# Kernel optimization log

Measured on AMD Instinct MI355X. Metric: run time of the kernel, lower is better.

The kernel has to match this reference:

```python
import jax, jax.numpy as jnp
import numpy as np

D_MODEL = 1024; D_STATE = 128; D_CONV = 4; EXPAND = 2; HEADDIM = 64; NGROUPS = 1
CHUNK = 256; B_SZ = 2; SEQ = 4096
D_INNER = EXPAND * D_MODEL
NHEADS = D_INNER // HEADDIM
CONV_DIM = D_INNER + 2 * NGROUPS * D_STATE
D_IN_PROJ = 2 * D_INNER + 2 * NGROUPS * D_STATE + NHEADS
EPS = 1e-5


def setup_inputs() -> dict:
    key = jax.random.key(0)
    ks = jax.random.split(key, 12)
    # dt_bias init exactly as in the module (inverse-softplus of dt in [dt_min, dt_max])
    dt0 = jnp.exp(jax.random.uniform(ks[0], (NHEADS,)) * (np.log(0.1) - np.log(0.001)) + np.log(0.001))
    dt0 = jnp.clip(dt0, 1e-4)
    dt_bias = dt0 + jnp.log(-jnp.expm1(-dt0))
    A_log = jnp.log(jax.random.uniform(ks[1], (NHEADS,), minval=1.0, maxval=16.0))
    return {
        "u": jax.random.normal(ks[2], (B_SZ, SEQ, D_MODEL), jnp.float32),
        "delta_t": jax.random.uniform(ks[3], (B_SZ, SEQ, 1), jnp.float32),
        "W_in": jax.random.normal(ks[4], (D_IN_PROJ, D_MODEL), jnp.float32) / np.sqrt(D_MODEL),
        "conv_w": jax.random.normal(ks[5], (CONV_DIM, D_CONV), jnp.float32) * 0.2,
        "conv_b": jax.random.normal(ks[6], (CONV_DIM,), jnp.float32) * 0.02,
        "dt_bias": dt_bias,
        "gamma": jax.random.uniform(ks[7], (NHEADS,)),
        "A_log": A_log,
        "D": jnp.ones((NHEADS,), jnp.float32),
        "norm_w": jnp.ones((D_INNER,), jnp.float32),
        "W_out": jax.random.normal(ks[8], (D_MODEL, D_INNER), jnp.float32) / np.sqrt(D_INNER),
    }


def _segsum(x):
    # x: (..., T) -> (..., T, T) masked lower-triangular segment sums
    T = x.shape[-1]
    cs = jnp.cumsum(x, axis=-1)
    seg = cs[..., :, None] - cs[..., None, :]
    mask = jnp.tril(jnp.ones((T, T), bool))
    return jnp.where(mask, seg, -jnp.inf)


def _forward(u, delta_t, W_in, conv_w, conv_b, dt_bias, gamma, A_log, D, norm_w, W_out):
    b, L, _ = u.shape
    zxbcdt = u @ W_in.T                               # (b, L, d_in_proj), d_mlp == 0
    z = zxbcdt[..., :D_INNER]
    xBC = zxbcdt[..., D_INNER:D_INNER + CONV_DIM]
    dt = zxbcdt[..., D_INNER + CONV_DIM:]             # (b, L, nheads)
    dt = dt + gamma[None, None, :] * delta_t          # time-scale-aware shift
    # causal depthwise conv1d (pad left d_conv-1) + SiLU
    xBC = jax.lax.conv_general_dilated(
        xBC.transpose(0, 2, 1), conv_w[:, None, :], (1,), [(D_CONV - 1, 0)],
        feature_group_count=CONV_DIM, dimension_numbers=("NCH", "OIH", "NCH"))
    xBC = jax.nn.silu(xBC.transpose(0, 2, 1) + conv_b)
    x = xBC[..., :D_INNER].reshape(b, L, NHEADS, HEADDIM)
    Bm = xBC[..., D_INNER:D_INNER + D_STATE]          # ngroups == 1 -> (b, L, n)
    Cm = xBC[..., D_INNER + D_STATE:]
    A = -jnp.exp(A_log)                               # (h,)
    dt = jax.nn.softplus(dt + dt_bias)                # dt_softplus=True, dt_limit=(0, inf)
    # ---- chunked SSD scan (mamba_chunk_scan_combined) ----
    c = L // CHUNK
    Xc = (x * dt[..., None]).reshape(b, c, CHUNK, NHEADS, HEADDIM)
    Ac = (dt * A).reshape(b, c, CHUNK, NHEADS).transpose(0, 3, 1, 2)    # (b,h,c,Q)
    Bc = Bm.reshape(b, c, CHUNK, D_STATE)
    Cc = Cm.reshape(b, c, CHUNK, D_STATE)
    A_cumsum = jnp.cumsum(Ac, axis=-1)                                   # (b,h,c,Q)
    Lmat = jnp.exp(_segsum(Ac))                                          # (b,h,c,Q,Q)
    # intra-chunk (diagonal blocks)
    Y_diag = jnp.einsum("bcqn,bckn,bhcqk,bckhp->bcqhp", Cc, Bc, Lmat, Xc)
    # per-chunk states at chunk ends
    decay_states = jnp.exp(A_cumsum[..., -1:] - A_cumsum)                # (b,h,c,Q)
    states = jnp.einsum("bckn,bhck,bckhp->bchpn", Bc, decay_states, Xc)
    # inter-chunk recurrence over chunk index
    chunk_decay = jnp.exp(A_cumsum[..., -1])                             # (b,h,c)

    def step(s, inp):
        dec, st = inp
        return dec[..., None, None] * s + st, s

    _, prev_states = jax.lax.scan(
        step,
        jnp.zeros((b, NHEADS, HEADDIM, D_STATE), Xc.dtype),
        (chunk_decay.transpose(2, 0, 1), states.transpose(1, 0, 2, 3, 4)))  # prev: (c,b,h,p,n)
    Y_off = jnp.einsum("bcqn,cbhpn,bhcq->bcqhp", Cc, prev_states, jnp.exp(A_cumsum))
    y = (Y_diag + Y_off).reshape(b, L, NHEADS, HEADDIM)
    y = y + x * D[None, None, :, None]                # skip connection D
    y = y.reshape(b, L, D_INNER)
    # gated RMSNorm (norm_before_gate=False): norm(y * silu(z)) * w, group_size = d_ssm
    yg = y * jax.nn.silu(z)
    yg = yg * jax.lax.rsqrt(jnp.mean(jnp.square(yg), axis=-1, keepdims=True) + EPS) * norm_w
    return yg @ W_out.T


def reference(u, delta_t, W_in, conv_w, conv_b, dt_bias, gamma, A_log, D, norm_w, W_out):
    return _forward(u, delta_t, W_in, conv_w, conv_b, dt_bias, gamma, A_log, D, norm_w, W_out)
```

## Files before the change

kernel.cpp:

```cpp
#include <hip/hip_runtime.h>
#include <hip/hip_bf16.h>
#include <math.h>

#define DM    1024
#define DIP   4384
#define NP1   4480
#define NPX   4352
#define DI    2048
#define CD    2304
#define NH    32
#define HD    64
#define DS    128
#define CH    256
#define NCH   16
#define BSZ   2
#define SEQ   4096
#define NTOK  (BSZ*SEQ)

typedef __bf16 bf16_t;
typedef __attribute__((ext_vector_type(8))) __bf16 bf16x8;
typedef __attribute__((ext_vector_type(4))) float f32x4;

__device__ __forceinline__ f32x4 mfma16(bf16x8 a, bf16x8 b, f32x4 c) {
    return __builtin_amdgcn_mfma_f32_16x16x32_bf16(a, b, c, 0, 0, 0);
}

__device__ __forceinline__ void gload_lds16(const bf16_t* g, bf16_t* l) {
    __builtin_amdgcn_global_load_lds(
        (const __attribute__((address_space(1))) unsigned int*)g,
        (__attribute__((address_space(3))) unsigned int*)l, 16, 0, 0);
}

__global__ void k_cvt(const float* __restrict__ in, bf16_t* __restrict__ out, int n) {
    int i = blockIdx.x * 256 + threadIdx.x;
    if (i < n) out[i] = (bf16_t)in[i];
}

__global__ void k_cvt_pad(const float* __restrict__ in, bf16_t* __restrict__ out) {
    int i = blockIdx.x * 256 + threadIdx.x;
    if (i >= NP1 * DM) return;
    int r = i >> 10;
    out[i] = (r < DIP) ? (bf16_t)in[i] : (bf16_t)0.f;
}

template <typename OutT>
__global__ __launch_bounds__(256) void k_gemm(const bf16_t* __restrict__ A,
                                              const bf16_t* __restrict__ Bt,
                                              OutT* __restrict__ C, int K, int ldc) {
    __shared__ __align__(16) bf16_t sA[128 * 32];
    __shared__ __align__(16) bf16_t sB[128 * 32];
    int tid = threadIdx.x, wave = tid >> 6, lane = tid & 63;
    int l15 = lane & 15, quad = lane >> 4;
    int m0 = blockIdx.y * 128, n0 = blockIdx.x * 128;
    int wm = (wave & 1) * 64, wn = (wave >> 1) * 64;
    f32x4 acc[4][4];
#pragma unroll
    for (int i = 0; i < 4; i++)
#pragma unroll
        for (int j = 0; j < 4; j++) acc[i][j] = (f32x4){0.f, 0.f, 0.f, 0.f};

    int srow = lane >> 2, scol = (lane & 3) * 8;
    const bf16_t* Ag0 = A + (size_t)(m0 + wave * 32 + srow) * K + scol;
    const bf16_t* Ag1 = Ag0 + (size_t)16 * K;
    const bf16_t* Bg0 = Bt + (size_t)(n0 + wave * 32 + srow) * K + scol;
    const bf16_t* Bg1 = Bg0 + (size_t)16 * K;
    bf16_t* lA0 = sA + (wave * 32) * 32;
    bf16_t* lA1 = sA + (wave * 32 + 16) * 32;
    bf16_t* lB0 = sB + (wave * 32) * 32;
    bf16_t* lB1 = sB + (wave * 32 + 16) * 32;

    for (int k0 = 0; k0 < K; k0 += 32) {
        gload_lds16(Ag0 + k0, lA0);
        gload_lds16(Ag1 + k0, lA1);
        gload_lds16(Bg0 + k0, lB0);
        gload_lds16(Bg1 + k0, lB1);
        __syncthreads();
        bf16x8 af[4], bg[4];
#pragma unroll
        for (int mt = 0; mt < 4; mt++) af[mt] = *(const bf16x8*)&sA[(wm + mt * 16 + l15) * 32 + quad * 8];
#pragma unroll
        for (int nt = 0; nt < 4; nt++) bg[nt] = *(const bf16x8*)&sB[(wn + nt * 16 + l15) * 32 + quad * 8];
#pragma unroll
        for (int mt = 0; mt < 4; mt++)
#pragma unroll
            for (int nt = 0; nt < 4; nt++)
                acc[mt][nt] = mfma16(af[mt], bg[nt], acc[mt][nt]);
        __syncthreads();
    }
#pragma unroll
    for (int mt = 0; mt < 4; mt++)
#pragma unroll
        for (int nt = 0; nt < 4; nt++)
#pragma unroll
            for (int r = 0; r < 4; r++)
                C[(size_t)(m0 + wm + mt * 16 + quad * 4 + r) * ldc + n0 + wn + nt * 16 + l15] =
                    (OutT)acc[mt][nt][r];
}

__global__ __launch_bounds__(256) void k_dtcum(const float* __restrict__ dtf,
                                               const float* __restrict__ delta_t,
                                               const float* __restrict__ gamma,
                                               const float* __restrict__ dt_bias,
                                               const float* __restrict__ A_log,
                                               float* __restrict__ dtb, float* __restrict__ acum) {
    int blk = blockIdx.x;
    int h = blk & (NH - 1), bc = blk >> 5;
    int q = threadIdx.x;
    size_t tok = (size_t)bc * CH + q;
    float x = dtf[tok * 128 + h] + gamma[h] * delta_t[tok] + dt_bias[h];
    float dt = (x > 20.f) ? x : log1pf(expf(x));
    float Ah = -expf(A_log[h]);
    __shared__ __align__(16) float s[CH];
    s[q] = dt * Ah;
    __syncthreads();
#pragma unroll
    for (int off = 1; off < CH; off <<= 1) {
        float v = (q >= off) ? s[q - off] : 0.f;
        __syncthreads();
        s[q] += v;
        __syncthreads();
    }
    dtb[(size_t)blk * CH + q] = dt;
    acum[(size_t)blk * CH + q] = s[q];
}

__global__ __launch_bounds__(256) void k_conv(const bf16_t* __restrict__ zxp,
                                              const float* __restrict__ cw,
                                              const float* __restrict__ cb,
                                              bf16_t* __restrict__ xBC) {
    int ch = blockIdx.x * 256 + threadIdx.x;
    int tok0 = blockIdx.y * 8;
    int l0 = tok0 & (SEQ - 1);
    float w0 = cw[ch * 4], w1 = cw[ch * 4 + 1], w2 = cw[ch * 4 + 2], w3 = cw[ch * 4 + 3];
    float bias = cb[ch];
    float h0 = 0.f, h1 = 0.f, h2 = 0.f;
    if (l0 != 0) {
        h0 = (float)zxp[(size_t)(tok0 - 3) * NPX + ch];
        h1 = (float)zxp[(size_t)(tok0 - 2) * NPX + ch];
        h2 = (float)zxp[(size_t)(tok0 - 1) * NPX + ch];
    }
#pragma unroll
    for (int j = 0; j < 8; j++) {
        float cur = (float)zxp[(size_t)(tok0 + j) * NPX + ch];
        float acc = bias + h0 * w0 + h1 * w1 + h2 * w2 + cur * w3;
        float sv = acc / (1.f + expf(-acc));
        xBC[(size_t)(tok0 + j) * CD + ch] = (bf16_t)sv;
        h0 = h1; h1 = h2; h2 = cur;
    }
}

__global__ __launch_bounds__(256) void k_trans(const bf16_t* __restrict__ xBC,
                                               const float* __restrict__ dtb,
                                               bf16_t* __restrict__ Xt, bf16_t* __restrict__ Btr) {
    int t = blockIdx.x, bc = blockIdx.y, tid = threadIdx.x;
    __shared__ __align__(16) bf16_t tile[CH][72];
    __shared__ __align__(16) float sdt[CH];
    int chbase = (t < 32) ? t * 64 : DI + (t - 32) * 64;
#pragma unroll
    for (int pp = 0; pp < 8; pp++) {
        int q = pp * 32 + (tid >> 3), col = (tid & 7) * 8;
        *(bf16x8*)&tile[q][col] = *(const bf16x8*)(xBC + (size_t)(bc * CH + q) * CD + chbase + col);
    }
    if (t < 32) sdt[tid] = dtb[(size_t)(bc * NH + t) * CH + tid];
    __syncthreads();
    int pl = tid >> 2, qg = tid & 3;
#pragma unroll
    for (int c8 = 0; c8 < 8; c8++) {
        int q0 = qg * 64 + c8 * 8;
        bf16x8 v;
        if (t < 32) {
#pragma unroll
            for (int j = 0; j < 8; j++) v[j] = (bf16_t)((float)tile[q0 + j][pl] * sdt[q0 + j]);
            size_t row = (size_t)(bc * NH + t) * 64 + pl;
            *(bf16x8*)(Xt + row * CH + q0) = v;
        } else {
#pragma unroll
            for (int j = 0; j < 8; j++) v[j] = tile[q0 + j][pl];
            size_t row = (size_t)bc * DS + (t - 32) * 64 + pl;
            *(bf16x8*)(Btr + row * CH + q0) = v;
        }
    }
}

__global__ __launch_bounds__(256) void k_states(const bf16_t* __restrict__ Xt,
                                                const bf16_t* __restrict__ Btr,
                                                const float* __restrict__ acum,
                                                float* __restrict__ states) {
    int blk = blockIdx.x;
    int bc = blk >> 5;
    int tid = threadIdx.x, wave = tid >> 6, lane = tid & 63;
    int l15 = lane & 15, quad = lane >> 4;
    __shared__ __align__(16) float sdec[CH];
    {
        size_t base = (size_t)blk * CH;
        float al = acum[base + CH - 1];
        sdec[tid] = expf(al - acum[base + tid]);
    }
    __syncthreads();
    const bf16_t* Xb = Xt + (size_t)blk * 64 * CH;
    const bf16_t* Bb = Btr + (size_t)bc * DS * CH;
    f32x4 acc[4][2];
#pragma unroll
    for (int i = 0; i < 4; i++)
#pragma unroll
        for (int j = 0; j < 2; j++) acc[i][j] = (f32x4){0.f, 0.f, 0.f, 0.f};
#pragma unroll
    for (int ks = 0; ks < 8; ks++) {
        float d0[8];
#pragma unroll
        for (int j = 0; j < 8; j++) d0[j] = sdec[ks * 32 + quad * 8 + j];
        bf16x8 a[4], b[2];
#pragma unroll
        for (int mt = 0; mt < 4; mt++) {
            bf16x8 raw = *(const bf16x8*)(Xb + (size_t)(mt * 16 + l15) * CH + ks * 32 + quad * 8);
#pragma unroll
            for (int j = 0; j < 8; j++) a[mt][j] = (bf16_t)((float)raw[j] * d0[j]);
        }
#pragma unroll
        for (int nt = 0; nt < 2; nt++)
            b[nt] = *(const bf16x8*)(Bb + (size_t)(wave * 32 + nt * 16 + l15) * CH + ks * 32 + quad * 8);
#pragma unroll
        for (int mt = 0; mt < 4; mt++)
#pragma unroll
            for (int nt = 0; nt < 2; nt++)
                acc[mt][nt] = mfma16(a[mt], b[nt], acc[mt][nt]);
    }
#pragma unroll
    for (int mt = 0; mt < 4; mt++)
#pragma unroll
        for (int nt = 0; nt < 2; nt++)
#pragma unroll
            for (int r = 0; r < 4; r++)
                states[(size_t)blk * 64 * DS + (size_t)(mt * 16 + quad * 4 + r) * DS + wave * 32 + nt * 16 + l15] = acc[mt][nt][r];
}

__global__ __launch_bounds__(256) void k_scan(const float* __restrict__ states,
                                              const float* __restrict__ acum,
                                              bf16_t* __restrict__ prevb) {
    int blk = blockIdx.x;
    int bh = blk >> 5;
    int b = bh >> 5, h = bh & 31;
    int e = (blk & 31) * 256 + threadIdx.x;
    float prev = 0.f;
    for (int c = 0; c < NCH; c++) {
        size_t idx = (size_t)(b * NCH + c) * NH + h;
        float dec = expf(acum[idx * CH + CH - 1]);
        size_t i = idx * 64 * DS + e;
        prevb[i] = (bf16_t)prev;
        prev = prev * dec + states[i];
    }
}

__global__ __launch_bounds__(256) void k_sgen(const bf16_t* __restrict__ xBC,
                                              bf16_t* __restrict__ Sraw) {
    int t = blockIdx.x, bc = blockIdx.y;
    int qt = (t == 0) ? 1 : (t < 3) ? 2 : 3;
    int kt = t - qt * (qt - 1) / 2;
    int tid = threadIdx.x, wave = tid >> 6, lane = tid & 63;
    int l15 = lane & 15, quad = lane >> 4;
    const bf16_t* Cbase = xBC + (size_t)bc * CH * CD + DI + DS;
    const bf16_t* Bbase = xBC + (size_t)bc * CH * CD + DI;
    f32x4 acc[4];
#pragma unroll
    for (int j = 0; j < 4; j++) acc[j] = (f32x4){0.f, 0.f, 0.f, 0.f};
#pragma unroll
    for (int ks = 0; ks < 4; ks++) {
        bf16x8 a = *(const bf16x8*)(Cbase + (size_t)(qt * 64 + wave * 16 + l15) * CD + ks * 32 + quad * 8);
        bf16x8 b[4];
#pragma unroll
        for (int nt = 0; nt < 4; nt++)
            b[nt] = *(const bf16x8*)(Bbase + (size_t)(kt * 64 + nt * 16 + l15) * CD + ks * 32 + quad * 8);
#pragma unroll
        for (int nt = 0; nt < 4; nt++) acc[nt] = mfma16(a, b[nt], acc[nt]);
    }
    bf16_t* out = Sraw + ((size_t)bc * 6 + t) * 64 * 64;
#pragma unroll
    for (int nt = 0; nt < 4; nt++)
#pragma unroll
        for (int r = 0; r < 4; r++)
            out[(size_t)(wave * 16 + quad * 4 + r) * 64 + nt * 16 + l15] = (bf16_t)acc[nt][r];
}

__global__ __launch_bounds__(256) void k_chunky(const bf16_t* __restrict__ xBC,
                                                const bf16_t* __restrict__ Xt,
                                                const bf16_t* __restrict__ prevb,
                                                const bf16_t* __restrict__ Sraw,
                                                const float* __restrict__ acum,
                                                const float* __restrict__ Dp,
                                                bf16_t* __restrict__ yf) {
    int blk = blockIdx.x;
    int bc = blk >> 5, h = blk & 31;
    int tid = threadIdx.x, wave = tid >> 6, lane = tid & 63;
    int l15 = lane & 15, quad = lane >> 4;
    __shared__ __align__(16) float sac[CH];
    __shared__ __align__(16) bf16_t sS[4][64][72];
    sac[tid] = acum[(size_t)blk * CH + tid];
    __syncthreads();

    const bf16_t* Cbase = xBC + (size_t)bc * CH * CD + DI + DS;
    const bf16_t* Bbase = xBC + (size_t)bc * CH * CD + DI;
    const bf16_t* XtB = Xt + (size_t)blk * 64 * CH;
    const bf16_t* pvB = prevb + (size_t)blk * 64 * DS;

    int qw = wave * 64;
    float refq = sac[qw];
    float s_ref = expf(refq);
    f32x4 acc[4][4];
#pragma unroll
    for (int i = 0; i < 4; i++)
#pragma unroll
        for (int j = 0; j < 4; j++) acc[i][j] = (f32x4){0.f, 0.f, 0.f, 0.f};

#pragma unroll
    for (int ks = 0; ks < 4; ks++) {
        bf16x8 a[4], b[4];
#pragma unroll
        for (int mt = 0; mt < 4; mt++)
            a[mt] = *(const bf16x8*)(Cbase + (size_t)(qw + mt * 16 + l15) * CD + ks * 32 + quad * 8);
#pragma unroll
        for (int nt = 0; nt < 4; nt++)
            b[nt] = *(const bf16x8*)(pvB + (size_t)(nt * 16 + l15) * DS + ks * 32 + quad * 8);
#pragma unroll
        for (int mt = 0; mt < 4; mt++)
#pragma unroll
            for (int nt = 0; nt < 4; nt++)
                acc[mt][nt] = mfma16(a[mt], b[nt], acc[mt][nt]);
    }
#pragma unroll
    for (int mt = 0; mt < 4; mt++)
#pragma unroll
        for (int nt = 0; nt < 4; nt++)
#pragma unroll
            for (int r = 0; r < 4; r++) acc[mt][nt][r] *= s_ref;

    for (int kt = 0; kt < wave; kt++) {
        const bf16_t* St = Sraw + ((size_t)bc * 6 + wave * (wave - 1) / 2 + kt) * 64 * 64;
#pragma unroll
        for (int ks = 0; ks < 2; ks++) {
            float ekv[8];
#pragma unroll
            for (int j = 0; j < 8; j++)
                ekv[j] = __expf(refq - sac[kt * 64 + ks * 32 + quad * 8 + j]);
            bf16x8 a[4], b[4];
#pragma unroll
            for (int mt = 0; mt < 4; mt++)
                a[mt] = *(const bf16x8*)(St + (size_t)(mt * 16 + l15) * 64 + ks * 32 + quad * 8);
#pragma unroll
            for (int nt = 0; nt < 4; nt++) {
                bf16x8 raw = *(const bf16x8*)(XtB + (size_t)(nt * 16 + l15) * CH + kt * 64 + ks * 32 + quad * 8);
#pragma unroll
                for (int j = 0; j < 8; j++) b[nt][j] = (bf16_t)((float)raw[j] * ekv[j]);
            }
#pragma unroll
            for (int mt = 0; mt < 4; mt++)
#pragma unroll
                for (int nt = 0; nt < 4; nt++)
                    acc[mt][nt] = mfma16(a[mt], b[nt], acc[mt][nt]);
        }
    }

    float sacq[4][4];
#pragma unroll
    for (int mt = 0; mt < 4; mt++)
#pragma unroll
        for (int r = 0; r < 4; r++) sacq[mt][r] = sac[qw + mt * 16 + quad * 4 + r];
#pragma unroll
    for (int mt = 0; mt < 4; mt++) {
        float eqv[4];
#pragma unroll
        for (int r = 0; r < 4; r++) eqv[r] = __expf(sacq[mt][r] - refq);
#pragma unroll
        for (int nt = 0; nt < 4; nt++)
#pragma unroll
            for (int r = 0; r < 4; r++) acc[mt][nt][r] *= eqv[r];
    }

    {
        int kt = wave;
        f32x4 s2[4][4];
#pragma unroll
        for (int i = 0; i < 4; i++)
#pragma unroll
            for (int j = 0; j < 4; j++) s2[i][j] = (f32x4){0.f, 0.f, 0.f, 0.f};
#pragma unroll
        for (int ks = 0; ks < 4; ks++) {
            bf16x8 a[4], b[4];
#pragma unroll
            for (int mt = 0; mt < 4; mt++)
                a[mt] = *(const bf16x8*)(Cbase + (size_t)(qw + mt * 16 + l15) * CD + ks * 32 + quad * 8);
#pragma unroll
            for (int nt = 0; nt < 4; nt++)
                b[nt] = *(const bf16x8*)(Bbase + (size_t)(kt * 64 + nt * 16 + l15) * CD + ks * 32 + quad * 8);
#pragma unroll
            for (int mt = 0; mt < 4; mt++)
#pragma unroll
                for (int nt = 0; nt < 4; nt++)
                    s2[mt][nt] = mfma16(a[mt], b[nt], s2[mt][nt]);
        }
        float sack[4];
#pragma unroll
        for (int nt = 0; nt < 4; nt++) sack[nt] = sac[kt * 64 + nt * 16 + l15];
#pragma unroll
        for (int mt = 0; mt < 4; mt++)
#pragma unroll
            for (int nt = 0; nt < 4; nt++) {
                int kp = kt * 64 + nt * 16 + l15;
#pragma unroll
                for (int r = 0; r < 4; r++) {
                    int lq = mt * 16 + quad * 4 + r;
                    int q = qw + lq;
                    float v = (kp <= q) ? s2[mt][nt][r] * __expf(sacq[mt][r] - sack[nt]) : 0.f;
                    sS[wave][lq][nt * 16 + l15] = (bf16_t)v;
                }
            }
#pragma unroll
        for (int ks = 0; ks < 2; ks++) {
            bf16x8 a[4], b[4];
#pragma unroll
            for (int mt = 0; mt < 4; mt++)
                a[mt] = *(const bf16x8*)&sS[wave][mt * 16 + l15][ks * 32 + quad * 8];
#pragma unroll
            for (int nt = 0; nt < 4; nt++)
                b[nt] = *(const bf16x8*)(XtB + (size_t)(nt * 16 + l15) * CH + kt * 64 + ks * 32 + quad * 8);
#pragma unroll
            for (int mt = 0; mt < 4; mt++)
#pragma unroll
                for (int nt = 0; nt < 4; nt++)
                    acc[mt][nt] = mfma16(a[mt], b[nt], acc[mt][nt]);
        }
    }

    float Dh = Dp[h];
#pragma unroll
    for (int mt = 0; mt < 4; mt++)
#pragma unroll
        for (int nt = 0; nt < 4; nt++)
#pragma unroll
            for (int r = 0; r < 4; r++) {
                int q = qw + mt * 16 + quad * 4 + r;
                int p = nt * 16 + l15;
                size_t tok = (size_t)bc * CH + q;
                float xv = (float)xBC[tok * CD + h * 64 + p];
                yf[tok * DI + h * 64 + p] = (bf16_t)(acc[mt][nt][r] + Dh * xv);
            }
}

__global__ __launch_bounds__(256) void k_gate(const bf16_t* __restrict__ yf,
                                              const bf16_t* __restrict__ zb,
                                              const float* __restrict__ nw,
                                              bf16_t* __restrict__ yg) {
    int tok = blockIdx.x, tid = threadIdx.x;
    float g[8];
    float ss = 0.f;
#pragma unroll
    for (int j = 0; j < 8; j++) {
        int d = tid + j * 256;
        float z = (float)zb[(size_t)tok * NPX + d];
        float yy = (float)yf[(size_t)tok * DI + d];
        float gg = yy * (z / (1.f + expf(-z)));
        g[j] = gg;
        ss += gg * gg;
    }
#pragma unroll
    for (int off = 32; off > 0; off >>= 1) ss += __shfl_down(ss, off);
    __shared__ __align__(16) float sw[4];
    int wave = tid >> 6, lane = tid & 63;
    if (lane == 0) sw[wave] = ss;
    __syncthreads();
    float tot = sw[0] + sw[1] + sw[2] + sw[3];
    float r = rsqrtf(tot / (float)DI + 1e-5f);
#pragma unroll
    for (int j = 0; j < 8; j++) {
        int d = tid + j * 256;
        yg[(size_t)tok * DI + d] = (bf16_t)(g[j] * r * nw[d]);
    }
}

extern "C" void kernel_launch(void* const* d_in, const int* in_sizes, int n_in,
                              void* d_out, int out_size, void* d_ws, size_t ws_size,
                              hipStream_t stream) {
    const float* u       = (const float*)d_in[0];
    const float* delta_t = (const float*)d_in[1];
    const float* W_in    = (const float*)d_in[2];
    const float* conv_w  = (const float*)d_in[3];
    const float* conv_b  = (const float*)d_in[4];
    const float* dt_bias = (const float*)d_in[5];
    const float* gamma   = (const float*)d_in[6];
    const float* A_log   = (const float*)d_in[7];
    const float* Dp      = (const float*)d_in[8];
    const float* norm_w  = (const float*)d_in[9];
    const float* W_out   = (const float*)d_in[10];
    float* out = (float*)d_out;

    char* p = (char*)d_ws;
    auto alloc = [&](size_t bytes) -> char* {
        char* r = p;
        p += (bytes + 255) & ~(size_t)255;
        return r;
    };
    bf16_t* zxBC    = (bf16_t*)alloc((size_t)NTOK * NPX * 2);
    bf16_t* Win_bf  = (bf16_t*)alloc((size_t)NP1 * DM * 2);
    bf16_t* Wout_bf = (bf16_t*)alloc((size_t)DM * DI * 2);
    float*  dtb     = (float*)alloc((size_t)NTOK * NH * 4);
    float*  acum    = (float*)alloc((size_t)NTOK * NH * 4);
    bf16_t* xBC_bf  = (bf16_t*)alloc((size_t)NTOK * CD * 2);
    bf16_t* Xt      = (bf16_t*)alloc((size_t)NTOK * DI * 2);
    bf16_t* poolA   = (bf16_t*)alloc((size_t)NTOK * DM * 2);
    bf16_t* Btr     = (bf16_t*)alloc((size_t)BSZ * NCH * DS * CH * 2);
    bf16_t* Sraw    = (bf16_t*)alloc((size_t)BSZ * NCH * 6 * 64 * 64 * 2);
    float*  dtf     = (float*)d_out;
    float*  states  = (float*)d_out;
    bf16_t* yf      = (bf16_t*)d_out;
    bf16_t* u_bf    = poolA;
    bf16_t* prevb   = poolA;
    bf16_t* yg_bf   = Xt;

    k_cvt<<<(NTOK * DM + 255) / 256, 256, 0, stream>>>(u, u_bf, NTOK * DM);
    k_cvt_pad<<<(NP1 * DM + 255) / 256, 256, 0, stream>>>(W_in, Win_bf);
    k_cvt<<<(DM * DI + 255) / 256, 256, 0, stream>>>(W_out, Wout_bf, DM * DI);

    k_gemm<bf16_t><<<dim3(NPX / 128, NTOK / 128), 256, 0, stream>>>(u_bf, Win_bf, zxBC, DM, NPX);
    k_gemm<float><<<dim3(1, NTOK / 128), 256, 0, stream>>>(u_bf, Win_bf + (size_t)NPX * DM, dtf, DM, 128);

    k_dtcum<<<BSZ * NCH * NH, CH, 0, stream>>>(dtf, delta_t, gamma, dt_bias, A_log, dtb, acum);
    k_conv<<<dim3(CD / 256, NTOK / 8), 256, 0, stream>>>(zxBC + DI, conv_w, conv_b, xBC_bf);
    k_sgen<<<dim3(6, BSZ * NCH), 256, 0, stream>>>(xBC_bf, Sraw);
    k_trans<<<dim3(34, BSZ * NCH), 256, 0, stream>>>(xBC_bf, dtb, Xt, Btr);
    k_states<<<BSZ * NCH * NH, 256, 0, stream>>>(Xt, Btr, acum, states);
    k_scan<<<BSZ * NH * 32, 256, 0, stream>>>(states, acum, prevb);
    k_chunky<<<BSZ * NCH * NH, 256, 0, stream>>>(xBC_bf, Xt, prevb, Sraw, acum, Dp, yf);
    k_gate<<<NTOK, 256, 0, stream>>>(yf, zxBC, norm_w, yg_bf);

    k_gemm<float><<<dim3(DM / 128, NTOK / 128), 256, 0, stream>>>(yg_bf, Wout_bf, out, DI, DM);
}
```

Before: 471.3 us.

## Swizzle GEMM LDS tiles, merge convert kernels, fuse chunk S-gemm loop, fast exp

The three fp32-to-bf16 conversion launches become one combined kernel. The GEMM LDS tile now uses an XOR swizzle of 16-byte chunks on both the global-to-LDS write and the fragment reads, to reduce bank conflicts. In k_chunky the C·B^T diagonal-block matmul is merged into the same k-loop as the C·prev_state matmul, so the C fragments are loaded once, at the cost of more live accumulator registers. Several expf calls become __expf, which is less accurate.

```diff
diff --git a/kernel.cpp b/kernel.cpp
--- a/kernel.cpp
+++ b/kernel.cpp
@@ -31,16 +31,24 @@
         (__attribute__((address_space(3))) unsigned int*)l, 16, 0, 0);
 }
 
-__global__ void k_cvt(const float* __restrict__ in, bf16_t* __restrict__ out, int n) {
+#define CVT_U   (NTOK * DM)
+#define CVT_WI  (NP1 * DM)
+#define CVT_WO  (DM * DI)
+__global__ void k_cvt_all(const float* __restrict__ u, const float* __restrict__ wi,
+                          const float* __restrict__ wo,
+                          bf16_t* __restrict__ u_bf, bf16_t* __restrict__ wi_bf,
+                          bf16_t* __restrict__ wo_bf) {
     int i = blockIdx.x * 256 + threadIdx.x;
-    if (i < n) out[i] = (bf16_t)in[i];
-}
-
-__global__ void k_cvt_pad(const float* __restrict__ in, bf16_t* __restrict__ out) {
-    int i = blockIdx.x * 256 + threadIdx.x;
-    if (i >= NP1 * DM) return;
-    int r = i >> 10;
-    out[i] = (r < DIP) ? (bf16_t)in[i] : (bf16_t)0.f;
+    if (i < CVT_U) {
+        u_bf[i] = (bf16_t)u[i];
+    } else if (i < CVT_U + CVT_WI) {
+        int j = i - CVT_U;
+        int r = j >> 10;
+        wi_bf[j] = (r < DIP) ? (bf16_t)wi[j] : (bf16_t)0.f;
+    } else if (i < CVT_U + CVT_WI + CVT_WO) {
+        int j = i - CVT_U - CVT_WI;
+        wo_bf[j] = (bf16_t)wo[j];
+    }
 }
 
 template <typename OutT>
@@ -59,7 +67,8 @@
 #pragma unroll
         for (int j = 0; j < 4; j++) acc[i][j] = (f32x4){0.f, 0.f, 0.f, 0.f};
 
-    int srow = lane >> 2, scol = (lane & 3) * 8;
+    int srow = lane >> 2, sc = lane & 3;
+    int scol = (sc ^ ((srow >> 1) & 3)) * 8;
     const bf16_t* Ag0 = A + (size_t)(m0 + wave * 32 + srow) * K + scol;
     const bf16_t* Ag1 = Ag0 + (size_t)16 * K;
     const bf16_t* Bg0 = Bt + (size_t)(n0 + wave * 32 + srow) * K + scol;
@@ -69,6 +78,8 @@
     bf16_t* lB0 = sB + (wave * 32) * 32;
     bf16_t* lB1 = sB + (wave * 32 + 16) * 32;
 
+    int rchunk = (quad ^ ((l15 >> 1) & 3)) * 8;
+
     for (int k0 = 0; k0 < K; k0 += 32) {
         gload_lds16(Ag0 + k0, lA0);
         gload_lds16(Ag1 + k0, lA1);
@@ -77,9 +88,9 @@
         __syncthreads();
         bf16x8 af[4], bg[4];
 #pragma unroll
-        for (int mt = 0; mt < 4; mt++) af[mt] = *(const bf16x8*)&sA[(wm + mt * 16 + l15) * 32 + quad * 8];
-#pragma unroll
-        for (int nt = 0; nt < 4; nt++) bg[nt] = *(const bf16x8*)&sB[(wn + nt * 16 + l15) * 32 + quad * 8];
+        for (int mt = 0; mt < 4; mt++) af[mt] = *(const bf16x8*)&sA[(wm + mt * 16 + l15) * 32 + rchunk];
+#pragma unroll
+        for (int nt = 0; nt < 4; nt++) bg[nt] = *(const bf16x8*)&sB[(wn + nt * 16 + l15) * 32 + rchunk];
 #pragma unroll
         for (int mt = 0; mt < 4; mt++)
 #pragma unroll
@@ -194,7 +205,7 @@
     {
         size_t base = (size_t)blk * CH;
         float al = acum[base + CH - 1];
-        sdec[tid] = expf(al - acum[base + tid]);
+        sdec[tid] = __expf(al - acum[base + tid]);
     }
     __syncthreads();
     const bf16_t* Xb = Xt + (size_t)blk * 64 * CH;
@@ -244,7 +255,7 @@
     float prev = 0.f;
     for (int c = 0; c < NCH; c++) {
         size_t idx = (size_t)(b * NCH + c) * NH + h;
-        float dec = expf(acum[idx * CH + CH - 1]);
+        float dec = __expf(acum[idx * CH + CH - 1]);
         size_t i = idx * 64 * DS + e;
         prevb[i] = (bf16_t)prev;
         prev = prev * dec + states[i];
@@ -304,27 +315,34 @@
 
     int qw = wave * 64;
     float refq = sac[qw];
-    float s_ref = expf(refq);
-    f32x4 acc[4][4];
+    float s_ref = __expf(refq);
+    f32x4 acc[4][4], s2[4][4];
 #pragma unroll
     for (int i = 0; i < 4; i++)
 #pragma unroll
-        for (int j = 0; j < 4; j++) acc[i][j] = (f32x4){0.f, 0.f, 0.f, 0.f};
+        for (int j = 0; j < 4; j++) {
+            acc[i][j] = (f32x4){0.f, 0.f, 0.f, 0.f};
+            s2[i][j] = (f32x4){0.f, 0.f, 0.f, 0.f};
+        }
 
 #pragma unroll
     for (int ks = 0; ks < 4; ks++) {
-        bf16x8 a[4], b[4];
+        bf16x8 a[4], bp[4], bb[4];
 #pragma unroll
         for (int mt = 0; mt < 4; mt++)
             a[mt] = *(const bf16x8*)(Cbase + (size_t)(qw + mt * 16 + l15) * CD + ks * 32 + quad * 8);
 #pragma unroll
-        for (int nt = 0; nt < 4; nt++)
-            b[nt] = *(const bf16x8*)(pvB + (size_t)(nt * 16 + l15) * DS + ks * 32 + quad * 8);
+        for (int nt = 0; nt < 4; nt++) {
+            bp[nt] = *(const bf16x8*)(pvB + (size_t)(nt * 16 + l15) * DS + ks * 32 + quad * 8);
+            bb[nt] = *(const bf16x8*)(Bbase + (size_t)(qw + nt * 16 + l15) * CD + ks * 32 + quad * 8);
+        }
 #pragma unroll
         for (int mt = 0; mt < 4; mt++)
 #pragma unroll
-            for (int nt = 0; nt < 4; nt++)
-                acc[mt][nt] = mfma16(a[mt], b[nt], acc[mt][nt]);
+            for (int nt = 0; nt < 4; nt++) {
+                acc[mt][nt] = mfma16(a[mt], bp[nt], acc[mt][nt]);
+                s2[mt][nt] = mfma16(a[mt], bb[nt], s2[mt][nt]);
+            }
     }
 #pragma unroll
     for (int mt = 0; mt < 4; mt++)
@@ -377,26 +395,6 @@
 
     {
         int kt = wave;
-        f32x4 s2[4][4];
-#pragma unroll
-        for (int i = 0; i < 4; i++)
-#pragma unroll
-            for (int j = 0; j < 4; j++) s2[i][j] = (f32x4){0.f, 0.f, 0.f, 0.f};
-#pragma unroll
-        for (int ks = 0; ks < 4; ks++) {
-            bf16x8 a[4], b[4];
-#pragma unroll
-            for (int mt = 0; mt < 4; mt++)
-                a[mt] = *(const bf16x8*)(Cbase + (size_t)(qw + mt * 16 + l15) * CD + ks * 32 + quad * 8);
-#pragma unroll
-            for (int nt = 0; nt < 4; nt++)
-                b[nt] = *(const bf16x8*)(Bbase + (size_t)(kt * 64 + nt * 16 + l15) * CD + ks * 32 + quad * 8);
-#pragma unroll
-            for (int mt = 0; mt < 4; mt++)
-#pragma unroll
-                for (int nt = 0; nt < 4; nt++)
-                    s2[mt][nt] = mfma16(a[mt], b[nt], s2[mt][nt]);
-        }
         float sack[4];
 #pragma unroll
         for (int nt = 0; nt < 4; nt++) sack[nt] = sac[kt * 64 + nt * 16 + l15];
@@ -515,9 +513,8 @@
     bf16_t* prevb   = poolA;
     bf16_t* yg_bf   = Xt;
 
-    k_cvt<<<(NTOK * DM + 255) / 256, 256, 0, stream>>>(u, u_bf, NTOK * DM);
-    k_cvt_pad<<<(NP1 * DM + 255) / 256, 256, 0, stream>>>(W_in, Win_bf);
-    k_cvt<<<(DM * DI + 255) / 256, 256, 0, stream>>>(W_out, Wout_bf, DM * DI);
+    k_cvt_all<<<(CVT_U + CVT_WI + CVT_WO + 255) / 256, 256, 0, stream>>>(
+        u, W_in, W_out, u_bf, Win_bf, Wout_bf);
 
     k_gemm<bf16_t><<<dim3(NPX / 128, NTOK / 128), 256, 0, stream>>>(u_bf, Win_bf, zxBC, DM, NPX);
     k_gemm<float><<<dim3(1, NTOK / 128), 256, 0, stream>>>(u_bf, Win_bf + (size_t)NPX * DM, dtf, DM, 128);
```

After: 488.4 us. +3.6%, slower.
